# Performance work log

Measured on AMD Instinct MI355X. Metric: run time of the kernel, lower is better.

## Reference

```python
import jax, jax.numpy as jnp
import numpy as np
import math

B, L, D, H, FF = 32, 512, 512, 8, 2048
DH = D // H
EPS = 1e-5

def pe_table(L, D):
    pos = jnp.arange(L, dtype=jnp.float32)[:, None]
    div = jnp.exp(jnp.arange(0, D, 2, dtype=jnp.float32) * (-(math.log(10000.0) / D)))
    pe = jnp.zeros((L, D), dtype=jnp.float32)
    pe = pe.at[:, 0::2].set(jnp.sin(pos * div))
    pe = pe.at[:, 1::2].set(jnp.cos(pos * div))
    return pe

def setup_inputs() -> dict:
    key = jax.random.key(0)
    ks = jax.random.split(key, 16)
    s = 0.02
    inp = {
        "x": jax.random.normal(ks[0], (B, L, D), jnp.float32),
        "mask": jnp.ones((B, L), jnp.int32),
        "speaker_emb": jax.random.normal(ks[1], (B, L, D), jnp.float32),
        "Wg": jax.random.normal(ks[2], (D, D), jnp.float32) * s,
        "Wq": jax.random.normal(ks[3], (D, D), jnp.float32) * s,
        "bq": jnp.zeros((D,), jnp.float32),
        "Wk": jax.random.normal(ks[4], (D, D), jnp.float32) * s,
        "bk": jnp.zeros((D,), jnp.float32),
        "Wv": jax.random.normal(ks[5], (D, D), jnp.float32) * s,
        "bv": jnp.zeros((D,), jnp.float32),
        "Wo": jax.random.normal(ks[6], (D, D), jnp.float32) * s,
        "bo": jnp.zeros((D,), jnp.float32),
        "ln_g": jnp.ones((D,), jnp.float32),
        "ln_b": jnp.zeros((D,), jnp.float32),
        "W1": jax.random.normal(ks[7], (FF, D), jnp.float32) * s,
        "b1": jnp.zeros((FF,), jnp.float32),
        "W2": jax.random.normal(ks[8], (D, FF), jnp.float32) * s,
        "b2": jnp.zeros((D,), jnp.float32),
    }
    return inp

def layer_norm(x, g, b):
    mu = jnp.mean(x, axis=-1, keepdims=True)
    var = jnp.var(x, axis=-1, keepdims=True)
    return (x - mu) * jax.lax.rsqrt(var + EPS) * g + b

def reference(x, mask, speaker_emb, Wg, Wq, bq, Wk, bk, Wv, bv, Wo, bo, ln_g, ln_b, W1, b1, W2, b2):
    # DynamicGating: sigmoid(x W^T) * x
    x = jax.nn.sigmoid(x @ Wg.T) * x
    # speaker embedding + sinusoidal positional encoding (dropout is eval/no-op)
    x = x + speaker_emb + pe_table(L, D)[None, :, :]
    # Multi-head self-attention (eager, full score matrix)
    q = (x @ Wq.T + bq).reshape(B, L, H, DH).transpose(0, 2, 1, 3) / math.sqrt(DH)
    k = (x @ Wk.T + bk).reshape(B, L, H, DH).transpose(0, 2, 1, 3)
    v = (x @ Wv.T + bv).reshape(B, L, H, DH).transpose(0, 2, 1, 3)
    scores = jnp.einsum("bhqd,bhkd->bhqk", q, k)  # (B,H,L,L)
    key_mask = (mask == 0)[:, None, None, :]  # mask keys where mask==0
    scores = jnp.where(key_mask, jnp.float32(-1e10), scores)
    attn = jax.nn.softmax(scores, axis=-1)
    ctx = jnp.einsum("bhqk,bhkd->bhqd", attn, v)
    ctx = ctx.transpose(0, 2, 1, 3).reshape(B, L, D)
    attn_out = ctx @ Wo.T + bo
    h = attn_out + x  # residual (dropout no-op)
    # FeedForwardNet: note GELU applied after BOTH linears (faithful to source)
    mid = jax.nn.gelu(layer_norm(h, ln_g, ln_b) @ W1.T + b1, approximate=True)
    out = jax.nn.gelu(mid @ W2.T + b2, approximate=True)
    return out + h
```

## Files before the change

### kernel.cpp

```cpp
#include <hip/hip_runtime.h>
#include <math.h>

#define Bn 32
#define Ln 512
#define Dn 512
#define Hn 8
#define DHn 64
#define FFn 2048
#define Mn (Bn*Ln)
#define QKVS 1536

typedef __attribute__((ext_vector_type(4))) float f32x4;
typedef __attribute__((ext_vector_type(8))) short short8;

__device__ __forceinline__ float bf2f(ushort u){ return __uint_as_float(((unsigned)u) << 16); }
__device__ __forceinline__ ushort f2bf(float f){
  unsigned u = __float_as_uint(f);
  u += 0x7FFFu + ((u >> 16) & 1u);
  return (ushort)(u >> 16);
}
__device__ __forceinline__ float gelu_fast(float x){
  float y2 = 1.5957691216057308f * (x + 0.044715f*x*x*x);
  return x / (1.0f + __expf(-y2));
}

__device__ __forceinline__ void gload_lds16(const ushort* g, ushort* l){
  __builtin_amdgcn_global_load_lds(
      (__attribute__((address_space(1))) void*)(void*)g,
      (__attribute__((address_space(3))) void*)(void*)l, 16, 0, 0);
}

__device__ __forceinline__ void cvt4(const float* __restrict__ in, ushort* __restrict__ out, int u){
  float4 v = *(const float4*)(in + u*4);
  ushort4 o;
  o.x = f2bf(v.x); o.y = f2bf(v.y); o.z = f2bf(v.z); o.w = f2bf(v.w);
  *(ushort4*)(out + u*4) = o;
}

__global__ __launch_bounds__(256) void prep_kernel(
    const float* __restrict__ Wg, const float* __restrict__ Wq, const float* __restrict__ Wk,
    const float* __restrict__ Wv, const float* __restrict__ Wo, const float* __restrict__ W1,
    const float* __restrict__ W2,
    const float* __restrict__ bq, const float* __restrict__ bk, const float* __restrict__ bv,
    ushort* __restrict__ wgb, ushort* __restrict__ wqkvb, ushort* __restrict__ wob,
    ushort* __restrict__ w1b, ushort* __restrict__ w2b,
    float* __restrict__ pe, float* __restrict__ bqkv)
{
  int u = blockIdx.x*256 + threadIdx.x;
  const int WU = 65536, FU = 262144;
  if (u < WU){ cvt4(Wg, wgb, u); return; }            u -= WU;
  if (u < WU){ cvt4(Wq, wqkvb, u); return; }          u -= WU;
  if (u < WU){ cvt4(Wk, wqkvb + 262144, u); return; } u -= WU;
  if (u < WU){ cvt4(Wv, wqkvb + 524288, u); return; } u -= WU;
  if (u < WU){ cvt4(Wo, wob, u); return; }            u -= WU;
  if (u < FU){ cvt4(W1, w1b, u); return; }            u -= FU;
  if (u < FU){ cvt4(W2, w2b, u); return; }            u -= FU;
  if (u < WU){
    int e = u*4; int l = e >> 9; int d0 = e & 511;
    #pragma unroll
    for (int p=0;p<2;p++){
      int i = (d0 >> 1) + p;
      float dv = expf((float)(2*i) * (-9.210340371976184f/512.0f));
      float ang = (float)l * dv;
      pe[e + 2*p]     = sinf(ang);
      pe[e + 2*p + 1] = cosf(ang);
    }
    return;
  }
  u -= WU;
  if (u < 384){
    int e = u*4;
    #pragma unroll
    for (int j=0;j<4;j++){
      int i = e + j;
      bqkv[i] = (i < 512) ? bq[i] : (i < 1024) ? bk[i-512] : bv[i-1024];
    }
  }
}

__global__ void cvt_kernel(const float* __restrict__ in, ushort* __restrict__ out, int n){
  int i = (blockIdx.x*256 + threadIdx.x)*4;
  if (i >= n) return;
  cvt4(in, out, i >> 2);
}

template<int MODE>
__global__ __launch_bounds__(512) void gemm_kernel(
    const ushort* __restrict__ A, const ushort* __restrict__ W,
    const float* __restrict__ bias,
    const float* __restrict__ res,
    const ushort* __restrict__ rbf,
    const float* __restrict__ spk, const float* __restrict__ pe,
    float* __restrict__ outf, ushort* __restrict__ outb, ushort* __restrict__ outb2,
    int K, int N, int gx)
{
  __shared__ ushort lbuf[3][24576];
  int t = threadIdx.x;
  int wave = t >> 6, lane = t & 63;
  int wrow = wave >> 2, wcol = wave & 3;
  int g = lane >> 4, r16 = lane & 15;

  int nwg = gx * (Mn/256);
  int wg = blockIdx.x;
  int tile = (wg & 7)*(nwg >> 3) + (wg >> 3);
  int trow = tile / gx;
  int tcol = tile - trow*gx;
  int rowBase = trow * 256;
  int colBase = tcol * 128;

  int srow8 = lane >> 3;
  int sucol = ((lane & 7) ^ srow8) * 8;
  const ushort* gA = A + (size_t)(rowBase + wave*8 + srow8)*K + sucol;
  const ushort* gW = W + (size_t)(colBase + wave*8 + srow8)*K + sucol;

  int NT = K >> 6;

  f32x4 acc[8][2];
  #pragma unroll
  for (int m=0;m<8;m++)
    #pragma unroll
    for (int n=0;n<2;n++) acc[m][n] = (f32x4)0.0f;

  #pragma unroll
  for (int c=0;c<4;c++) gload_lds16(gA + (size_t)c*64*K,      &lbuf[0][c*4096 + wave*512]);
  #pragma unroll
  for (int c=0;c<2;c++) gload_lds16(gW + (size_t)c*64*K,      &lbuf[0][16384 + c*4096 + wave*512]);
  #pragma unroll
  for (int c=0;c<4;c++) gload_lds16(gA + (size_t)c*64*K + 64, &lbuf[1][c*4096 + wave*512]);
  #pragma unroll
  for (int c=0;c<2;c++) gload_lds16(gW + (size_t)c*64*K + 64, &lbuf[1][16384 + c*4096 + wave*512]);
  asm volatile("s_waitcnt vmcnt(6)" ::: "memory");
  __builtin_amdgcn_s_barrier();

  int cur = 0, stg = 2;
  for (int kt = 0; kt < NT; ++kt){
    if (kt + 2 < NT){
      int k0 = (kt + 2) << 6;
      #pragma unroll
      for (int c=0;c<4;c++) gload_lds16(gA + (size_t)c*64*K + k0, &lbuf[stg][c*4096 + wave*512]);
      #pragma unroll
      for (int c=0;c<2;c++) gload_lds16(gW + (size_t)c*64*K + k0, &lbuf[stg][16384 + c*4096 + wave*512]);
    }
    const ushort* ab = &lbuf[cur][0];
    const ushort* bb = &lbuf[cur][16384];
    __builtin_amdgcn_s_setprio(1);
    #pragma unroll
    for (int ks=0; ks<2; ks++){
      short8 af[8], bfr[2];
      #pragma unroll
      for (int m=0;m<8;m++){
        int row = wrow*128 + m*16 + r16;
        af[m] = *(const short8*)&ab[row*64 + (((ks<<2)+g) ^ (row & 7))*8];
      }
      #pragma unroll
      for (int n=0;n<2;n++){
        int row = wcol*32 + n*16 + r16;
        bfr[n] = *(const short8*)&bb[row*64 + (((ks<<2)+g) ^ (row & 7))*8];
      }
      #pragma unroll
      for (int m=0;m<8;m++)
        #pragma unroll
        for (int n=0;n<2;n++)
          acc[m][n] = __builtin_amdgcn_mfma_f32_16x16x32_bf16(af[m], bfr[n], acc[m][n], 0, 0, 0);
    }
    __builtin_amdgcn_s_setprio(0);
    if (kt + 1 < NT){
      if (kt + 2 < NT) asm volatile("s_waitcnt vmcnt(6)" ::: "memory");
      else             asm volatile("s_waitcnt vmcnt(0)" ::: "memory");
      __builtin_amdgcn_s_barrier();
    }
    cur = (cur == 2) ? 0 : cur + 1;
    stg = (stg == 2) ? 0 : stg + 1;
  }

  if constexpr (MODE == 0 || MODE == 1 || MODE == 3){
    bool vpart = false;
    if constexpr (MODE == 1) vpart = (colBase >= 1024);
    if (!vpart){
      __syncthreads();
      ushort* ct = &lbuf[0][0];
      #pragma unroll
      for (int m=0;m<8;m++){
        #pragma unroll
        for (int n=0;n<2;n++){
          int col = wcol*32 + n*16 + r16;
          int gc = colBase + col;
          float sc = 1.0f;
          if constexpr (MODE == 1) sc = (gc < 512) ? 0.125f : 1.0f;
          #pragma unroll
          for (int j=0;j<4;j++){
            int row = wrow*128 + m*16 + g*4 + j;
            float c = acc[m][n][j];
            ushort val;
            if constexpr (MODE == 0){
              int gr = rowBase + row;
              size_t o = (size_t)gr * N + gc;
              float s = 1.0f/(1.0f + __expf(-c));
              val = f2bf(s * res[o] + spk[o] + pe[(gr & (Ln-1))*Dn + gc]);
            } else if constexpr (MODE == 3){
              val = f2bf(gelu_fast(c + bias[gc]));
            } else {
              val = f2bf((c + bias[gc]) * sc);
            }
            ct[row*128 + (col ^ ((row & 7) << 3))] = val;
          }
        }
      }
      __syncthreads();
      int r = t >> 1, ch = (t & 1)*64;
      ushort* dst = outb + (size_t)(rowBase + r)*N + colBase + ch;
      #pragma unroll
      for (int q=0;q<8;q++){
        int col = (ch + q*8) ^ ((r & 7) << 3);
        *(short8*)(dst + q*8) = *(const short8*)&ct[r*128 + col];
      }
    } else {
      #pragma unroll
      for (int m=0;m<8;m++){
        #pragma unroll
        for (int n=0;n<2;n++){
          int gc = colBase + wcol*32 + n*16 + r16;
          int dhg = gc - 1024;
          int gr0 = rowBase + wrow*128 + m*16 + g*4;
          int bb2 = gr0 >> 9, l0 = gr0 & 511;
          ushort4 o4;
          o4.x = f2bf(acc[m][n][0] + bias[gc]);
          o4.y = f2bf(acc[m][n][1] + bias[gc]);
          o4.z = f2bf(acc[m][n][2] + bias[gc]);
          o4.w = f2bf(acc[m][n][3] + bias[gc]);
          *(ushort4*)(outb2 + ((size_t)(bb2*Hn + (dhg>>6))*DHn + (dhg & 63))*Ln + l0) = o4;
        }
      }
    }
  } else {
    #pragma unroll
    for (int m=0;m<8;m++){
      #pragma unroll
      for (int n=0;n<2;n++){
        int gc = colBase + wcol*32 + n*16 + r16;
        #pragma unroll
        for (int j=0;j<4;j++){
          int gr = rowBase + wrow*128 + m*16 + g*4 + j;
          size_t o = (size_t)gr * N + gc;
          float c = acc[m][n][j];
          if constexpr (MODE == 2){
            outf[o] = c + bias[gc] + bf2f(rbf[o]);
          } else {
            outf[o] = gelu_fast(c + bias[gc]) + res[o];
          }
        }
      }
    }
  }
}

__global__ __launch_bounds__(256) void attn_mfma_kernel(
    const ushort* __restrict__ qb, const ushort* __restrict__ kb, const ushort* __restrict__ vtb,
    const int* __restrict__ mask, ushort* __restrict__ ctxb)
{
  __shared__ ushort lK[2][64][72];
  __shared__ ushort lVt[2][64][72];
  __shared__ ushort lP[4][32][72];

  int t = threadIdx.x;
  int w = t >> 6, lane = t & 63;
  int g = lane >> 4, r16 = lane & 15;
  int b = blockIdx.z, h = blockIdx.y;
  int qbase = blockIdx.x*128 + w*32;

  int key0 = t >> 3;
  int c8s = (t & 7) * 8;
  const ushort* kbase = kb + (size_t)(b*Ln)*QKVS + h*DHn + c8s;
  const ushort* vt = vtb + (size_t)((b*Hn + h)*DHn) * Ln;

  short8 af_q[2][2];
  #pragma unroll
  for (int m=0;m<2;m++)
    #pragma unroll
    for (int ks=0;ks<2;ks++)
      af_q[m][ks] = *(const short8*)(qb + (size_t)(b*Ln + qbase + m*16 + r16)*QKVS + h*DHn + ks*32 + g*8);

  f32x4 acc_ctx[2][4];
  #pragma unroll
  for (int m=0;m<2;m++)
    #pragma unroll
    for (int n=0;n<4;n++) acc_ctx[m][n] = (f32x4)0.0f;
  float mrun[2][4], lrun[2][4];
  #pragma unroll
  for (int m=0;m<2;m++)
    #pragma unroll
    for (int j=0;j<4;j++){ mrun[m][j] = -INFINITY; lrun[m][j] = 0.0f; }

  {
    short8 ka = *(const short8*)(kbase + (size_t)key0*QKVS);
    short8 kc = *(const short8*)(kbase + (size_t)(key0+32)*QKVS);
    short8 va = *(const short8*)(vt + (size_t)key0*Ln + c8s);
    short8 vc = *(const short8*)(vt + (size_t)(key0+32)*Ln + c8s);
    *(short8*)&lK[0][key0][c8s] = ka;
    *(short8*)&lK[0][key0+32][c8s] = kc;
    *(short8*)&lVt[0][key0][c8s] = va;
    *(short8*)&lVt[0][key0+32][c8s] = vc;
  }
  __syncthreads();
  int cb = 0;

  for (int kb0 = 0; kb0 < Ln; kb0 += 64){
    short8 kna, knb, vna, vnb;
    bool more = (kb0 + 64 < Ln);
    if (more){
      kna = *(const short8*)(kbase + (size_t)(kb0 + 64 + key0)*QKVS);
      knb = *(const short8*)(kbase + (size_t)(kb0 + 64 + key0 + 32)*QKVS);
      vna = *(const short8*)(vt + (size_t)key0*Ln + kb0 + 64 + c8s);
      vnb = *(const short8*)(vt + (size_t)(key0+32)*Ln + kb0 + 64 + c8s);
    }

    f32x4 acc_s[2][4];
    #pragma unroll
    for (int m=0;m<2;m++)
      #pragma unroll
      for (int n=0;n<4;n++) acc_s[m][n] = (f32x4)0.0f;
    __builtin_amdgcn_s_setprio(1);
    #pragma unroll
    for (int ks=0;ks<2;ks++){
      short8 bf_k[4];
      #pragma unroll
      for (int n=0;n<4;n++)
        bf_k[n] = *(const short8*)&lK[cb][n*16 + r16][ks*32 + g*8];
      #pragma unroll
      for (int m=0;m<2;m++)
        #pragma unroll
        for (int n=0;n<4;n++)
          acc_s[m][n] = __builtin_amdgcn_mfma_f32_16x16x32_bf16(af_q[m][ks], bf_k[n], acc_s[m][n], 0, 0, 0);
    }
    __builtin_amdgcn_s_setprio(0);

    #pragma unroll
    for (int n=0;n<4;n++){
      if (mask[b*Ln + kb0 + n*16 + r16] == 0){
        #pragma unroll
        for (int m=0;m<2;m++)
          #pragma unroll
          for (int j=0;j<4;j++) acc_s[m][n][j] = -1e10f;
      }
    }

    #pragma unroll
    for (int m=0;m<2;m++){
      #pragma unroll
      for (int j=0;j<4;j++){
        float tmax = fmaxf(fmaxf(acc_s[m][0][j], acc_s[m][1][j]),
                           fmaxf(acc_s[m][2][j], acc_s[m][3][j]));
        #pragma unroll
        for (int off=1; off<16; off<<=1) tmax = fmaxf(tmax, __shfl_xor(tmax, off));
        float newm = fmaxf(mrun[m][j], tmax);
        float alpha = __expf(mrun[m][j] - newm);
        float p0 = __expf(acc_s[m][0][j] - newm);
        float p1 = __expf(acc_s[m][1][j] - newm);
        float p2 = __expf(acc_s[m][2][j] - newm);
        float p3 = __expf(acc_s[m][3][j] - newm);
        float tsum = (p0+p1)+(p2+p3);
        #pragma unroll
        for (int off=1; off<16; off<<=1) tsum += __shfl_xor(tsum, off);
        lrun[m][j] = lrun[m][j]*alpha + tsum;
        mrun[m][j] = newm;
        #pragma unroll
        for (int n2=0;n2<4;n2++) acc_ctx[m][n2][j] *= alpha;
        int prow = m*16 + g*4 + j;
        lP[w][prow][0*16 + r16] = f2bf(p0);
        lP[w][prow][1*16 + r16] = f2bf(p1);
        lP[w][prow][2*16 + r16] = f2bf(p2);
        lP[w][prow][3*16 + r16] = f2bf(p3);
      }
    }

    __builtin_amdgcn_s_setprio(1);
    #pragma unroll
    for (int ks2=0;ks2<2;ks2++){
      short8 af_p[2], bf_v[4];
      #pragma unroll
      for (int m=0;m<2;m++)
        af_p[m] = *(const short8*)&lP[w][m*16 + r16][ks2*32 + g*8];
      #pragma unroll
      for (int n=0;n<4;n++)
        bf_v[n] = *(const short8*)&lVt[cb][n*16 + r16][ks2*32 + g*8];
      #pragma unroll
      for (int m=0;m<2;m++)
        #pragma unroll
        for (int n=0;n<4;n++)
          acc_ctx[m][n] = __builtin_amdgcn_mfma_f32_16x16x32_bf16(af_p[m], bf_v[n], acc_ctx[m][n], 0, 0, 0);
    }
    __builtin_amdgcn_s_setprio(0);

    if (more){
      *(short8*)&lK[cb^1][key0][c8s] = kna;
      *(short8*)&lK[cb^1][key0+32][c8s] = knb;
      *(short8*)&lVt[cb^1][key0][c8s] = vna;
      *(short8*)&lVt[cb^1][key0+32][c8s] = vnb;
    }
    __syncthreads();
    cb ^= 1;
  }

  #pragma unroll
  for (int m=0;m<2;m++){
    #pragma unroll
    for (int j=0;j<4;j++){
      float inv = 1.0f / lrun[m][j];
      int gr = qbase + m*16 + g*4 + j;
      #pragma unroll
      for (int n=0;n<4;n++){
        ctxb[(size_t)(b*Ln + gr)*Dn + h*DHn + n*16 + r16] = f2bf(acc_ctx[m][n][j] * inv);
      }
    }
  }
}

__global__ __launch_bounds__(256) void ln_kernel(
    const float* __restrict__ hbuf, const float* __restrict__ gamma, const float* __restrict__ beta,
    ushort* __restrict__ out)
{
  int row = blockIdx.x*4 + (threadIdx.x >> 6);
  int lane = threadIdx.x & 63;
  const float* p = hbuf + (size_t)row*Dn + lane*8;
  float4 a = *(const float4*)p;
  float4 c = *(const float4*)(p + 4);
  float v[8] = {a.x,a.y,a.z,a.w,c.x,c.y,c.z,c.w};
  float s = 0.f, ss = 0.f;
  #pragma unroll
  for (int j=0;j<8;j++){ s += v[j]; ss += v[j]*v[j]; }
  #pragma unroll
  for (int off=32; off>0; off>>=1){ s += __shfl_xor(s, off); ss += __shfl_xor(ss, off); }
  float mu = s * (1.0f/Dn);
  float var = ss * (1.0f/Dn) - mu*mu;
  float rstd = rsqrtf(var + 1e-5f);
  ushort o8[8];
  #pragma unroll
  for (int j=0;j<8;j++) o8[j] = f2bf((v[j]-mu)*rstd*gamma[lane*8+j] + beta[lane*8+j]);
  ushort* op = out + (size_t)row*Dn + lane*8;
  *(ushort4*)op       = make_ushort4(o8[0],o8[1],o8[2],o8[3]);
  *(ushort4*)(op + 4) = make_ushort4(o8[4],o8[5],o8[6],o8[7]);
}

extern "C" void kernel_launch(void* const* d_in, const int* in_sizes, int n_in,
                              void* d_out, int out_size, void* d_ws, size_t ws_size,
                              hipStream_t stream) {
  (void)in_sizes; (void)n_in; (void)out_size; (void)ws_size;
  const float* x    = (const float*)d_in[0];
  const int*   mask = (const int*)d_in[1];
  const float* spk  = (const float*)d_in[2];
  const float* Wg   = (const float*)d_in[3];
  const float* Wq   = (const float*)d_in[4];  const float* bq = (const float*)d_in[5];
  const float* Wk   = (const float*)d_in[6];  const float* bk = (const float*)d_in[7];
  const float* Wv   = (const float*)d_in[8];  const float* bv = (const float*)d_in[9];
  const float* Wo   = (const float*)d_in[10]; const float* bo = (const float*)d_in[11];
  const float* lng  = (const float*)d_in[12]; const float* lnbeta = (const float*)d_in[13];
  const float* W1   = (const float*)d_in[14]; const float* b1 = (const float*)d_in[15];
  const float* W2   = (const float*)d_in[16]; const float* b2 = (const float*)d_in[17];
  float* out = (float*)d_out;

  char* w = (char*)d_ws;
  size_t o = 0;
  ushort* xbf   = (ushort*)(w + o); o += (size_t)Mn*Dn*2;
  ushort* xinb  = (ushort*)(w + o); o += (size_t)Mn*Dn*2;
  ushort* qkvb  = (ushort*)(w + o); o += (size_t)Mn*QKVS*2;
  ushort* vtb   = (ushort*)(w + o); o += (size_t)Mn*Dn*2;
  ushort* ctxb  = (ushort*)(w + o); o += (size_t)Mn*Dn*2;
  float*  hbuf  = (float*)(w + o);  o += (size_t)Mn*Dn*4;
  ushort* lnbuf = (ushort*)(w + o); o += (size_t)Mn*Dn*2;
  ushort* wgb   = (ushort*)(w + o); o += (size_t)Dn*Dn*2;
  ushort* wqkvb = (ushort*)(w + o); o += (size_t)QKVS*Dn*2;
  ushort* wob   = (ushort*)(w + o); o += (size_t)Dn*Dn*2;
  ushort* w1b   = (ushort*)(w + o); o += (size_t)FFn*Dn*2;
  ushort* w2b   = (ushort*)(w + o); o += (size_t)Dn*FFn*2;
  float*  pebuf = (float*)(w + o);  o += (size_t)Ln*Dn*4;
  float*  bqkv  = (float*)(w + o);  o += (size_t)QKVS*4;
  ushort* midb  = xbf;

  hipLaunchKernelGGL(prep_kernel, dim3(3586), dim3(256), 0, stream,
                     Wg, Wq, Wk, Wv, Wo, W1, W2, bq, bk, bv,
                     wgb, wqkvb, wob, w1b, w2b, pebuf, bqkv);
  hipLaunchKernelGGL(cvt_kernel, dim3((Mn*Dn/4)/256), dim3(256), 0, stream, x, xbf, Mn*Dn);

  hipLaunchKernelGGL((gemm_kernel<0>), dim3((Dn/128)*(Mn/256)), dim3(512), 0, stream,
                     xbf, wgb, (const float*)nullptr, x, (const ushort*)nullptr, spk, pebuf,
                     (float*)nullptr, xinb, (ushort*)nullptr, Dn, Dn, Dn/128);
  hipLaunchKernelGGL((gemm_kernel<1>), dim3((QKVS/128)*(Mn/256)), dim3(512), 0, stream,
                     xinb, wqkvb, bqkv, (const float*)nullptr, (const ushort*)nullptr,
                     (const float*)nullptr, (const float*)nullptr,
                     (float*)nullptr, qkvb, vtb, Dn, QKVS, QKVS/128);
  hipLaunchKernelGGL(attn_mfma_kernel, dim3(Ln/128, Hn, Bn), dim3(256), 0, stream,
                     qkvb, qkvb + 512, vtb, mask, ctxb);
  hipLaunchKernelGGL((gemm_kernel<2>), dim3((Dn/128)*(Mn/256)), dim3(512), 0, stream,
                     ctxb, wob, bo, (const float*)nullptr, xinb, (const float*)nullptr,
                     (const float*)nullptr, hbuf, (ushort*)nullptr, (ushort*)nullptr, Dn, Dn, Dn/128);
  hipLaunchKernelGGL(ln_kernel, dim3(Mn/4), dim3(256), 0, stream, hbuf, lng, lnbeta, lnbuf);
  hipLaunchKernelGGL((gemm_kernel<3>), dim3((FFn/128)*(Mn/256)), dim3(512), 0, stream,
                     lnbuf, w1b, b1, (const float*)nullptr, (const ushort*)nullptr,
                     (const float*)nullptr, (const float*)nullptr,
                     (float*)nullptr, midb, (ushort*)nullptr, Dn, FFn, FFn/128);
  hipLaunchKernelGGL((gemm_kernel<4>), dim3((Dn/128)*(Mn/256)), dim3(512), 0, stream,
                     midb, w2b, b2, hbuf, (const ushort*)nullptr,
                     (const float*)nullptr, (const float*)nullptr,
                     out, (ushort*)nullptr, (ushort*)nullptr, FFn, Dn, Dn/128);
}
```

Before: 324.0 us.

## Split GEMM k-tile into two phases interleaving prefetch loads with MFMA

The GEMM main loop now handles each 64-wide k-tile in two explicit halves. Each half loads its LDS fragments, issues part of the next stage's global-to-LDS prefetch, then synchronises and runs its MFMAs under raised priority. Scheduling barriers pin the instruction order. The goal is to spread global loads between compute phases and keep waves in lockstep, so MFMA work overlaps memory traffic better. The cost is extra s_barrier calls per tile, which could add sync overhead.

New measurement: 324.3 us. No clear change (+0.1%).

```diff
diff --git a/kernel.cpp b/kernel.cpp
--- a/kernel.cpp
+++ b/kernel.cpp
@@ -131,44 +131,75 @@
   for (int c=0;c<2;c++) gload_lds16(gW + (size_t)c*64*K + 64, &lbuf[1][16384 + c*4096 + wave*512]);
   asm volatile("s_waitcnt vmcnt(6)" ::: "memory");
   __builtin_amdgcn_s_barrier();
+  __builtin_amdgcn_sched_barrier(0);
 
   int cur = 0, stg = 2;
   for (int kt = 0; kt < NT; ++kt){
-    if (kt + 2 < NT){
-      int k0 = (kt + 2) << 6;
-      #pragma unroll
-      for (int c=0;c<4;c++) gload_lds16(gA + (size_t)c*64*K + k0, &lbuf[stg][c*4096 + wave*512]);
-      #pragma unroll
-      for (int c=0;c<2;c++) gload_lds16(gW + (size_t)c*64*K + k0, &lbuf[stg][16384 + c*4096 + wave*512]);
-    }
     const ushort* ab = &lbuf[cur][0];
     const ushort* bb = &lbuf[cur][16384];
-    __builtin_amdgcn_s_setprio(1);
-    #pragma unroll
-    for (int ks=0; ks<2; ks++){
+    bool stage = (kt + 2 < NT);
+    int k0 = (kt + 2) << 6;
+
+    {
       short8 af[8], bfr[2];
       #pragma unroll
       for (int m=0;m<8;m++){
         int row = wrow*128 + m*16 + r16;
-        af[m] = *(const short8*)&ab[row*64 + (((ks<<2)+g) ^ (row & 7))*8];
+        af[m] = *(const short8*)&ab[row*64 + ((g ^ (row & 7)))*8];
       }
       #pragma unroll
       for (int n=0;n<2;n++){
         int row = wcol*32 + n*16 + r16;
-        bfr[n] = *(const short8*)&bb[row*64 + (((ks<<2)+g) ^ (row & 7))*8];
-      }
+        bfr[n] = *(const short8*)&bb[row*64 + ((g ^ (row & 7)))*8];
+      }
+      if (stage){
+        #pragma unroll
+        for (int c=0;c<3;c++) gload_lds16(gA + (size_t)c*64*K + k0, &lbuf[stg][c*4096 + wave*512]);
+      }
+      __builtin_amdgcn_s_barrier();
+      __builtin_amdgcn_s_setprio(1);
       #pragma unroll
       for (int m=0;m<8;m++)
         #pragma unroll
         for (int n=0;n<2;n++)
           acc[m][n] = __builtin_amdgcn_mfma_f32_16x16x32_bf16(af[m], bfr[n], acc[m][n], 0, 0, 0);
-    }
-    __builtin_amdgcn_s_setprio(0);
-    if (kt + 1 < NT){
-      if (kt + 2 < NT) asm volatile("s_waitcnt vmcnt(6)" ::: "memory");
-      else             asm volatile("s_waitcnt vmcnt(0)" ::: "memory");
+      __builtin_amdgcn_s_setprio(0);
       __builtin_amdgcn_s_barrier();
-    }
+      __builtin_amdgcn_sched_barrier(0);
+    }
+
+    {
+      short8 af[8], bfr[2];
+      #pragma unroll
+      for (int m=0;m<8;m++){
+        int row = wrow*128 + m*16 + r16;
+        af[m] = *(const short8*)&ab[row*64 + (((4 + g) ^ (row & 7)))*8];
+      }
+      #pragma unroll
+      for (int n=0;n<2;n++){
+        int row = wcol*32 + n*16 + r16;
+        bfr[n] = *(const short8*)&bb[row*64 + (((4 + g) ^ (row & 7)))*8];
+      }
+      if (stage){
+        gload_lds16(gA + (size_t)3*64*K + k0, &lbuf[stg][3*4096 + wave*512]);
+        #pragma unroll
+        for (int c=0;c<2;c++) gload_lds16(gW + (size_t)c*64*K + k0, &lbuf[stg][16384 + c*4096 + wave*512]);
+      }
+      if (stage)              asm volatile("s_waitcnt vmcnt(6)" ::: "memory");
+      else if (kt + 1 < NT)   asm volatile("s_waitcnt vmcnt(0)" ::: "memory");
+      __builtin_amdgcn_sched_barrier(0);
+      __builtin_amdgcn_s_barrier();
+      __builtin_amdgcn_s_setprio(1);
+      #pragma unroll
+      for (int m=0;m<8;m++)
+        #pragma unroll
+        for (int n=0;n<2;n++)
+          acc[m][n] = __builtin_amdgcn_mfma_f32_16x16x32_bf16(af[m], bfr[n], acc[m][n], 0, 0, 0);
+      __builtin_amdgcn_s_setprio(0);
+      __builtin_amdgcn_s_barrier();
+      __builtin_amdgcn_sched_barrier(0);
+    }
+
     cur = (cur == 2) ? 0 : cur + 1;
     stg = (stg == 2) ? 0 : stg + 1;
   }
```
